# Optimization experiments

Hardware: AMD Instinct MI355X
Metric: run time of the kernel (lower is better)

Reference implementation:

```python
import jax, jax.numpy as jnp
import numpy as np

N_STEPS = 2
MAX_STEP = 1.0
EPS64 = float(np.finfo(np.float64).eps)


def _sphere_log(p, q):
    # log map on unit sphere, tangent at p pointing to q; p,q: [..., D]
    cos = jnp.clip(jnp.sum(p * q, axis=-1, keepdims=True), -1.0, 1.0)
    u = q - cos * p
    un = jnp.linalg.norm(u, axis=-1, keepdims=True)
    theta = jnp.arccos(cos)
    return theta * u / (un + 1e-12)


def _sphere_exp(p, v):
    # exp map on unit sphere; jnp.sinc(n/pi) = sin(n)/n (stable at 0)
    n = jnp.linalg.norm(v, axis=-1, keepdims=True)
    x = jnp.cos(n) * p + jnp.sinc(n / jnp.pi) * v
    return x / jnp.linalg.norm(x, axis=-1, keepdims=True)


def setup_inputs() -> dict:
    key = jax.random.key(0)
    ks = jax.random.split(key, 6)
    N, C, D, E = 50000, 16, 3, 1600000
    nodes = jax.random.normal(ks[0], (N, C, D), dtype=jnp.float32)
    nodes = nodes / jnp.linalg.norm(nodes, axis=-1, keepdims=True)  # points on S^2
    edge_w = jax.random.uniform(ks[1], (E,), dtype=jnp.float32)
    senders = jax.random.randint(ks[2], (E,), 0, N, dtype=jnp.int32)
    receivers = jax.random.randint(ks[3], (E,), 0, N, dtype=jnp.int32)
    t_sqrt = 1.0 + 0.3 * jax.random.normal(ks[4], (C,), dtype=jnp.float32)
    delta_sqrt = 1.0 + 0.3 * jax.random.normal(ks[5], (C,), dtype=jnp.float32)
    return {"nodes": nodes, "edge_w": edge_w, "t_sqrt": t_sqrt,
            "delta_sqrt": delta_sqrt, "senders": senders, "receivers": receivers}


def reference(nodes, edge_w, t_sqrt, delta_sqrt, senders, receivers):
    N = nodes.shape[0]
    t = (t_sqrt ** 2) / N_STEPS            # per-channel time, split across Euler steps
    delta = delta_sqrt ** 2                 # per-channel min step size
    deg = jax.ops.segment_sum(edge_w, senders, num_segments=N)  # [N]

    def laplace(x):
        # graph Laplacian of manifold-valued signal: weighted mean of log maps, negated
        logs = _sphere_log(x[senders], x[receivers])              # [E, C, D]
        agg = jax.ops.segment_sum(edge_w[:, None, None] * logs, senders, num_segments=N)
        return -agg / (deg[:, None, None] + 1e-12)                # [N, C, D]

    def step(x, _):
        v = laplace(x)
        nrm = jnp.sqrt(jnp.sum(v * v, axis=-1) + EPS64)           # [N, C]
        alp = jax.nn.sigmoid(nrm - delta[None, :])
        scale = jnp.where(nrm * alp <= MAX_STEP, alp, MAX_STEP / nrm)
        v = -(v * scale[..., None]) * t[None, :, None]
        return _sphere_exp(x, v), None

    x, _ = jax.lax.scan(step, nodes, None, length=N_STEPS, unroll=N_STEPS)
    return x
```

## Files before the change

kernel.cpp:

```cpp
#include <hip/hip_runtime.h>
#include <math.h>


constexpr float EPS64F = 2.2204460492503131e-16f;
constexpr float PI_F   = 3.14159265358979323846f;
constexpr int   SR_BITS = 14;
constexpr int   CH_BITS = 15;

typedef int      vi4 __attribute__((ext_vector_type(4)));
typedef float    vf4 __attribute__((ext_vector_type(4)));
typedef float    vf2 __attribute__((ext_vector_type(2)));
typedef _Float16 vh4 __attribute__((ext_vector_type(4)));


__global__ __launch_bounds__(256) void lhist_kernel(
    const int* __restrict__ snd, unsigned char* __restrict__ pos,
    unsigned char* __restrict__ partial2, int E, int NC) {
  __shared__ int h[1 << SR_BITS];
  int tid = threadIdx.x;
  int c = blockIdx.x, s = blockIdx.y;
  for (int i = tid; i < (1 << SR_BITS); i += 256) h[i] = 0;
  __syncthreads();
  int base = c << CH_BITS;
  int cnt = min(1 << CH_BITS, E - base);
  int s0 = s << SR_BITS;
  const vi4* snd4 = (const vi4*)(snd + base);
  int cnt4 = cnt >> 2;
  for (int i = tid; i < cnt4; i += 256) {
    vi4 sv = snd4[i];
    int e = base + (i << 2);
    int v;
    v = sv.x - s0; if ((unsigned)v < (1u << SR_BITS)) pos[e]     = (unsigned char)atomicAdd(&h[v], 1);
    v = sv.y - s0; if ((unsigned)v < (1u << SR_BITS)) pos[e + 1] = (unsigned char)atomicAdd(&h[v], 1);
    v = sv.z - s0; if ((unsigned)v < (1u << SR_BITS)) pos[e + 2] = (unsigned char)atomicAdd(&h[v], 1);
    v = sv.w - s0; if ((unsigned)v < (1u << SR_BITS)) pos[e + 3] = (unsigned char)atomicAdd(&h[v], 1);
  }
  if (tid == 0) {
    for (int i = cnt4 << 2; i < cnt; ++i) {
      int v = snd[base + i] - s0;
      if ((unsigned)v < (1u << SR_BITS))
        pos[base + i] = (unsigned char)atomicAdd(&h[v], 1);
    }
  }
  __syncthreads();
  unsigned char* dst = partial2 + ((size_t)(s * NC + c) << SR_BITS);
  for (int i = tid; i < (1 << SR_BITS); i += 256)
    dst[i] = (unsigned char)h[i];
}

__global__ __launch_bounds__(1024) void scan1A_kernel(
    const unsigned char* __restrict__ partial2, unsigned char* __restrict__ boffL,
    int* __restrict__ row_start, int* __restrict__ btot, int N, int NC) {
  __shared__ int wsum[16];
  int tid = threadIdx.x;
  int lane = tid & 63, wave = tid >> 6;
  int i = blockIdx.x * 1024 + tid;
  int vpad = 0;
  if (i < N) {
    int s = i >> SR_BITS, lv = i & ((1 << SR_BITS) - 1);
    int run = 0;
    for (int c = 0; c < NC; ++c) {
      int t = partial2[((size_t)(s * NC + c) << SR_BITS) + lv];
      boffL[(size_t)c * N + i] = (unsigned char)run;
      run += t;
    }
    vpad = (run + 15) & ~15;
  }
  int incl = vpad;
  #pragma unroll
  for (int off = 1; off < 64; off <<= 1) {
    int t = __shfl_up(incl, off, 64);
    if (lane >= off) incl += t;
  }
  if (lane == 63) wsum[wave] = incl;
  __syncthreads();
  if (wave == 0 && lane < 16) {
    int wincl = wsum[lane];
    #pragma unroll
    for (int off = 1; off < 16; off <<= 1) {
      int t = __shfl_up(wincl, off, 64);
      if (lane >= off) wincl += t;
    }
    wsum[lane] = wincl;
  }
  __syncthreads();
  int woff = (wave > 0) ? wsum[wave - 1] : 0;
  if (i < N) row_start[i] = woff + incl - vpad;
  if (tid == 0) btot[blockIdx.x] = wsum[15];
}

__global__ __launch_bounds__(256) void scanCD_kernel(
    int* __restrict__ row_start, const int* __restrict__ btot,
    const float* __restrict__ nodes, vh4* __restrict__ nodes_h4,
    int N, int nb) {
  __shared__ int bsh[64];
  int tid = threadIdx.x;
  if (tid < 64) {
    int v = (tid < nb) ? btot[tid] : 0;
    int incl = v;
    #pragma unroll
    for (int off = 1; off < 64; off <<= 1) {
      int t = __shfl_up(incl, off, 64);
      if (tid >= off) incl += t;
    }
    bsh[tid] = incl - v;
    if (blockIdx.x == 0 && tid == 63) row_start[N] = incl;
  }
  __syncthreads();
  int i = blockIdx.x * 256 + tid;
  if (i < N) row_start[i] = row_start[i] + bsh[i >> 10];
  int total = N * 16;
  for (int idx = blockIdx.x * 256 + tid; idx < total; idx += gridDim.x * 256) {
    const float* s = nodes + idx * 3;
    vh4 h = {(_Float16)s[0], (_Float16)s[1], (_Float16)s[2], (_Float16)0.f};
    nodes_h4[idx] = h;
  }
}

__global__ __launch_bounds__(256) void fill_kernel(
    const vi4* __restrict__ snd4, const vi4* __restrict__ rcv4,
    const vf4* __restrict__ ew4, const unsigned char* __restrict__ pos,
    const unsigned char* __restrict__ boffL, const int* __restrict__ row_start,
    int* __restrict__ pair,
    const int* __restrict__ snd, const int* __restrict__ rcv,
    const float* __restrict__ ew, int N, int E) {
  int tid = threadIdx.x;
  int E4 = E >> 2;
  #pragma unroll
  for (int gg = 0; gg < 2; ++gg) {
    int g = blockIdx.x * 512 + gg * 256 + tid;
    if (g < E4) {
      int e = g << 2;
      const unsigned char* bc = boffL + (size_t)(e >> CH_BITS) * N;
      vi4 s = __builtin_nontemporal_load(&snd4[g]);
      vi4 r = __builtin_nontemporal_load(&rcv4[g]);
      vf4 w = __builtin_nontemporal_load(&ew4[g]);
      unsigned pb = *(const unsigned*)(pos + e);
      int rs0 = row_start[s.x] + bc[s.x];
      int rs1 = row_start[s.y] + bc[s.y];
      int rs2 = row_start[s.z] + bc[s.z];
      int rs3 = row_start[s.w] + bc[s.w];
      unsigned e0 = ((unsigned)(int)fmaf(w.x, 32767.f, 0.5f) << 17) | (unsigned)r.x;
      unsigned e1 = ((unsigned)(int)fmaf(w.y, 32767.f, 0.5f) << 17) | (unsigned)r.y;
      unsigned e2 = ((unsigned)(int)fmaf(w.z, 32767.f, 0.5f) << 17) | (unsigned)r.z;
      unsigned e3 = ((unsigned)(int)fmaf(w.w, 32767.f, 0.5f) << 17) | (unsigned)r.w;
      pair[rs0 + (pb & 255u)]         = (int)e0;
      pair[rs1 + ((pb >> 8) & 255u)]  = (int)e1;
      pair[rs2 + ((pb >> 16) & 255u)] = (int)e2;
      pair[rs3 + (pb >> 24)]          = (int)e3;
    }
  }
  if (blockIdx.x == 0 && tid == 0) {
    for (int e = E4 << 2; e < E; ++e) {
      int sn = snd[e];
      pair[row_start[sn] + boffL[(size_t)(e >> CH_BITS) * N + sn] + pos[e]] =
          (int)(((unsigned)(int)fmaf(ew[e], 32767.f, 0.5f) << 17) | (unsigned)rcv[e]);
    }
  }
}


__device__ __forceinline__ void edge_accum_pk(
    vf2 p0, vf2 p1, vf2 p2, vf2 q0, vf2 q1, vf2 q2, vf2 w,
    vf2& a0, vf2& a1, vf2& a2) {
  vf2 cs = p0 * q0 + p1 * q1 + p2 * q2;
  cs = __builtin_elementwise_min(vf2{1.f, 1.f},
       __builtin_elementwise_max(vf2{-1.f, -1.f}, cs));
  vf2 u0 = q0 - cs * p0;
  vf2 u1 = q1 - cs * p1;
  vf2 u2 = q2 - cs * p2;
  vf2 un2 = __builtin_elementwise_max(u0 * u0 + u1 * u1 + u2 * u2,
                                      vf2{1e-24f, 1e-24f});
  vf2 ax = __builtin_elementwise_abs(cs);
  vf2 s = __builtin_elementwise_sqrt(vf2{1.f, 1.f} - ax);
  vf2 poly = ((ax * -0.0187293f + 0.0742610f) * ax - 0.2121144f) * ax
             + 1.5707288f;
  vf2 th = s * poly;
  vf2 theta;
  theta.x = (cs.x >= 0.0f) ? th.x : (PI_F - th.x);
  theta.y = (cs.y >= 0.0f) ? th.y : (PI_F - th.y);
  vf2 rsq;
  rsq.x = __builtin_amdgcn_rsqf(un2.x);
  rsq.y = __builtin_amdgcn_rsqf(un2.y);
  vf2 coef = w * theta * rsq;
  a0 += coef * u0;
  a1 += coef * u1;
  a2 += coef * u2;
}

__device__ __forceinline__ void node_step(
    float a0, float a1, float a2, float ws, float p0, float p1, float p2,
    float ts, float dsv, float& y0, float& y1, float& y2) {
  float invdg = __builtin_amdgcn_rcpf(ws + 1e-12f);
  float g0 = a0 * invdg, g1 = a1 * invdg, g2 = a2 * invdg;
  float nrm = sqrtf(fmaf(g0, g0, fmaf(g1, g1, g2 * g2)) + EPS64F);
  float tch = ts * ts * 0.5f;
  float dch = dsv * dsv;
  float alp = __builtin_amdgcn_rcpf(1.0f + __expf(dch - nrm));
  float scale = (nrm * alp <= 1.0f) ? alp : __builtin_amdgcn_rcpf(nrm);
  float f = scale * tch;
  float v0 = g0 * f, v1 = g1 * f, v2 = g2 * f;
  float nv = sqrtf(fmaf(v0, v0, fmaf(v1, v1, v2 * v2)));
  float cn = __cosf(nv);
  float sc = (nv > 1e-20f) ? (__sinf(nv) * __builtin_amdgcn_rcpf(nv)) : 1.0f;
  float t0 = fmaf(cn, p0, sc * v0);
  float t1 = fmaf(cn, p1, sc * v1);
  float t2 = fmaf(cn, p2, sc * v2);
  float inv = __builtin_amdgcn_rsqf(fmaf(t0, t0, fmaf(t1, t1, t2 * t2)));
  y0 = t0 * inv; y1 = t1 * inv; y2 = t2 * inv;
}

__global__ __launch_bounds__(256, 8) void flowp_kernel(
    const vh4* __restrict__ xh4, const float* __restrict__ pf,
    const int* __restrict__ row_start, const int* __restrict__ pair,
    const float* __restrict__ tsq, const float* __restrict__ dsq,
    float* __restrict__ of, vh4* __restrict__ oh4, int N) {
  int node = blockIdx.x * 4 + (threadIdx.x >> 6);
  if (node >= N) return;
  int lane = threadIdx.x & 63;
  int c = lane & 15;
  int k = lane >> 4;
  int c3 = c * 3;
  int beg = row_start[node];
  int end = row_start[node + 1];
  int ip = node * 48 + c3;
  float ps0 = pf[ip], ps1 = pf[ip + 1], ps2 = pf[ip + 2];
  vf2 p0 = {ps0, ps0}, p1 = {ps1, ps1}, p2 = {ps2, ps2};
  vf2 a0 = {0.f, 0.f}, a1 = {0.f, 0.f}, a2 = {0.f, 0.f}, wsv = {0.f, 0.f};
  int iters = (end - beg) >> 4;
  int j = beg + k;
  constexpr float WS = 1.0f / 32767.0f;
  for (int t = 0; t < iters; ++t, j += 16) {
    int e0 = __builtin_nontemporal_load(&pair[j]);
    int e1 = __builtin_nontemporal_load(&pair[j + 4]);
    int e2 = __builtin_nontemporal_load(&pair[j + 8]);
    int e3 = __builtin_nontemporal_load(&pair[j + 12]);
    float w0 = (float)((unsigned)e0 >> 17) * WS;
    float w1 = (float)((unsigned)e1 >> 17) * WS;
    float w2 = (float)((unsigned)e2 >> 17) * WS;
    float w3 = (float)((unsigned)e3 >> 17) * WS;
    vh4 qva = xh4[((e0 & 0x1FFFF) << 4) + c];
    vh4 qvb = xh4[((e1 & 0x1FFFF) << 4) + c];
    vh4 qvc = xh4[((e2 & 0x1FFFF) << 4) + c];
    vh4 qvd = xh4[((e3 & 0x1FFFF) << 4) + c];
    float qa0 = (float)qva.x, qa1 = (float)qva.y, qa2 = (float)qva.z;
    float qb0 = (float)qvb.x, qb1 = (float)qvb.y, qb2 = (float)qvb.z;
    float qc0 = (float)qvc.x, qc1 = (float)qvc.y, qc2 = (float)qvc.z;
    float qd0 = (float)qvd.x, qd1 = (float)qvd.y, qd2 = (float)qvd.z;
    vf2 wA = {w0, w1}, wB = {w2, w3};
    edge_accum_pk(p0, p1, p2, vf2{qa0, qb0}, vf2{qa1, qb1},
                  vf2{qa2, qb2}, wA, a0, a1, a2);
    edge_accum_pk(p0, p1, p2, vf2{qc0, qd0}, vf2{qc1, qd1},
                  vf2{qc2, qd2}, wB, a0, a1, a2);
    wsv += wA + wB;
  }
  float A0 = a0.x + a0.y, A1 = a1.x + a1.y, A2 = a2.x + a2.y;
  float ws = wsv.x + wsv.y;
  A0 += __shfl_xor(A0, 16); A1 += __shfl_xor(A1, 16);
  A2 += __shfl_xor(A2, 16); ws += __shfl_xor(ws, 16);
  A0 += __shfl_xor(A0, 32); A1 += __shfl_xor(A1, 32);
  A2 += __shfl_xor(A2, 32); ws += __shfl_xor(ws, 32);
  if (k == 0) {
    float y0, y1, y2;
    node_step(A0, A1, A2, ws, ps0, ps1, ps2, tsq[c], dsq[c], y0, y1, y2);
    of[ip] = y0; of[ip + 1] = y1; of[ip + 2] = y2;
    if (oh4) {
      vh4 h = {(_Float16)y0, (_Float16)y1, (_Float16)y2, (_Float16)0.f};
      oh4[node * 16 + c] = h;
    }
  }
}

static inline size_t al16(size_t x) { return (x + 15) & ~(size_t)15; }

extern "C" void kernel_launch(void* const* d_in, const int* in_sizes, int n_in,
                              void* d_out, int out_size, void* d_ws, size_t ws_size,
                              hipStream_t stream) {
  const float* nodes = (const float*)d_in[0];
  const float* ew    = (const float*)d_in[1];
  const float* tsq   = (const float*)d_in[2];
  const float* dsq   = (const float*)d_in[3];
  const int*   snd   = (const int*)d_in[4];
  const int*   rcv   = (const int*)d_in[5];
  float* out = (float*)d_out;

  int E = in_sizes[1];
  int N = in_sizes[0] / 48;

  int NS = (N + (1 << SR_BITS) - 1) >> SR_BITS;
  int NC = (E + (1 << CH_BITS) - 1) >> CH_BITS;

  size_t padN  = (size_t)E + 15 * (size_t)N + 64;
  size_t rsB   = al16((size_t)(N + 4) * 4);
  size_t auxB  = 512;
  size_t pairB = al16(padN * 4);
  size_t p2B   = al16((size_t)NS * NC << SR_BITS);
  size_t xh4B  = al16((size_t)N * 16 * 8);
  size_t boffB = al16((size_t)NC * N * 4);
  if (p2B + boffB < 2 * xh4B) boffB = 2 * xh4B - p2B;

  char* base = (char*)d_ws;
  int*           row_start = (int*)base;
  int*           btot      = (int*)(base + rsB);
  int*           pair      = (int*)(base + rsB + auxB);
  unsigned char* partial2  = (unsigned char*)(base + rsB + auxB + pairB);
  unsigned char* boffL     = partial2 + p2B;
  unsigned char* pos       = boffL + boffB;
  vh4*           xtmp_h4   = (vh4*)partial2;
  vh4*           nodes_h4  = (vh4*)(partial2 + xh4B);

  int E4  = E >> 2;
  int nb  = (N + 1023) / 1024;
  int nb2 = (N + 255) / 256;
  int fbk = (E4 + 511) / 512;
  int nfb = (N + 3) / 4;

  hipMemsetAsync(pair, 0, pairB, stream);
  lhist_kernel<<<dim3(NC, NS), 256, 0, stream>>>(snd, pos, partial2, E, NC);
  scan1A_kernel<<<nb, 1024, 0, stream>>>(partial2, boffL, row_start, btot, N, NC);
  scanCD_kernel<<<nb2, 256, 0, stream>>>(row_start, btot, nodes, nodes_h4, N, nb);
  fill_kernel<<<fbk, 256, 0, stream>>>((const vi4*)snd, (const vi4*)rcv,
                                       (const vf4*)ew, pos, boffL, row_start,
                                       pair, snd, rcv, ew, N, E);

  flowp_kernel<<<nfb, 256, 0, stream>>>(nodes_h4, nodes, row_start, pair,
                                        tsq, dsq, out, xtmp_h4, N);
  flowp_kernel<<<nfb, 256, 0, stream>>>(xtmp_h4, out, row_start, pair,
                                        tsq, dsq, out, nullptr, N);
}
```

Measured before the change: 270.9 us.

## Merge preprocessing kernels, shrink CSR padding, encode weights as fp16

Drops the separate memset and scanCD launches. Pair zeroing and the fp16 node conversion move into the histogram kernel, and the block-offset scan moves into the last block of scan1A through an atomic ticket. Consumers add bshG per 1024-node block instead of using rewritten row_start. Row padding falls from 16 to 8, and the flow kernel now processes 2 edges per iteration instead of 4. Edge weights are packed as fp16 with a 16-bit receiver index, which limits N to 65536, and unroll 2 compensates for the smaller loop body.

After: 285.2 us. 5.3% more time.

```diff
diff --git a/kernel.cpp b/kernel.cpp
--- a/kernel.cpp
+++ b/kernel.cpp
@@ -15,7 +15,10 @@
 
 __global__ __launch_bounds__(256) void lhist_kernel(
     const int* __restrict__ snd, unsigned char* __restrict__ pos,
-    unsigned char* __restrict__ partial2, int E, int NC) {
+    unsigned char* __restrict__ partial2, int E, int NC,
+    vi4* __restrict__ pairz, int pairW4,
+    const float* __restrict__ nodes, vh4* __restrict__ nodes_h4,
+    int N, int* __restrict__ ticket) {
   __shared__ int h[1 << SR_BITS];
   int tid = threadIdx.x;
   int c = blockIdx.x, s = blockIdx.y;
@@ -46,11 +49,24 @@
   unsigned char* dst = partial2 + ((size_t)(s * NC + c) << SR_BITS);
   for (int i = tid; i < (1 << SR_BITS); i += 256)
     dst[i] = (unsigned char)h[i];
+  int lb = blockIdx.y * gridDim.x + blockIdx.x;
+  int nthr = gridDim.x * gridDim.y * 256;
+  int gtid = lb * 256 + tid;
+  if (gtid == 0) *ticket = 0;
+  vi4 z = {0, 0, 0, 0};
+  for (int i = gtid; i < pairW4; i += nthr) pairz[i] = z;
+  int total = N * 16;
+  for (int idx = gtid; idx < total; idx += nthr) {
+    const float* sp = nodes + idx * 3;
+    vh4 hh = {(_Float16)sp[0], (_Float16)sp[1], (_Float16)sp[2], (_Float16)0.f};
+    nodes_h4[idx] = hh;
+  }
 }
 
 __global__ __launch_bounds__(1024) void scan1A_kernel(
     const unsigned char* __restrict__ partial2, unsigned char* __restrict__ boffL,
-    int* __restrict__ row_start, int* __restrict__ btot, int N, int NC) {
+    int* __restrict__ row_start, int* __restrict__ btot,
+    int* __restrict__ ticket, int* __restrict__ bshG, int N, int NC) {
   __shared__ int wsum[16];
   int tid = threadIdx.x;
   int lane = tid & 63, wave = tid >> 6;
@@ -64,7 +80,7 @@
       boffL[(size_t)c * N + i] = (unsigned char)run;
       run += t;
     }
-    vpad = (run + 15) & ~15;
+    vpad = (run + 7) & ~7;
   }
   int incl = vpad;
   #pragma unroll
@@ -85,35 +101,26 @@
   }
   __syncthreads();
   int woff = (wave > 0) ? wsum[wave - 1] : 0;
-  if (i < N) row_start[i] = woff + incl - vpad;
+  if (i <= N) row_start[i] = woff + incl - vpad;
   if (tid == 0) btot[blockIdx.x] = wsum[15];
-}
-
-__global__ __launch_bounds__(256) void scanCD_kernel(
-    int* __restrict__ row_start, const int* __restrict__ btot,
-    const float* __restrict__ nodes, vh4* __restrict__ nodes_h4,
-    int N, int nb) {
-  __shared__ int bsh[64];
-  int tid = threadIdx.x;
-  if (tid < 64) {
-    int v = (tid < nb) ? btot[tid] : 0;
-    int incl = v;
-    #pragma unroll
-    for (int off = 1; off < 64; off <<= 1) {
-      int t = __shfl_up(incl, off, 64);
-      if (tid >= off) incl += t;
-    }
-    bsh[tid] = incl - v;
-    if (blockIdx.x == 0 && tid == 63) row_start[N] = incl;
-  }
-  __syncthreads();
-  int i = blockIdx.x * 256 + tid;
-  if (i < N) row_start[i] = row_start[i] + bsh[i >> 10];
-  int total = N * 16;
-  for (int idx = blockIdx.x * 256 + tid; idx < total; idx += gridDim.x * 256) {
-    const float* s = nodes + idx * 3;
-    vh4 h = {(_Float16)s[0], (_Float16)s[1], (_Float16)s[2], (_Float16)0.f};
-    nodes_h4[idx] = h;
+  __threadfence();
+  __shared__ int lastFlag;
+  if (tid == 0) lastFlag = (atomicAdd(ticket, 1) == (int)gridDim.x - 1);
+  __syncthreads();
+  if (lastFlag) {
+    __threadfence();
+    if (tid < 64) {
+      int nbk = (int)gridDim.x;
+      int v = (tid < nbk) ? ((volatile int*)btot)[tid] : 0;
+      int ic = v;
+      #pragma unroll
+      for (int off = 1; off < 64; off <<= 1) {
+        int t = __shfl_up(ic, off, 64);
+        if (tid >= off) ic += t;
+      }
+      bshG[tid] = ic - v;
+    }
+    if (tid == 0 && (N & 1023) == 0) row_start[N] = 0;
   }
 }
 
@@ -121,7 +128,7 @@
     const vi4* __restrict__ snd4, const vi4* __restrict__ rcv4,
     const vf4* __restrict__ ew4, const unsigned char* __restrict__ pos,
     const unsigned char* __restrict__ boffL, const int* __restrict__ row_start,
-    int* __restrict__ pair,
+    const int* __restrict__ bshG, int* __restrict__ pair,
     const int* __restrict__ snd, const int* __restrict__ rcv,
     const float* __restrict__ ew, int N, int E) {
   int tid = threadIdx.x;
@@ -136,14 +143,14 @@
       vi4 r = __builtin_nontemporal_load(&rcv4[g]);
       vf4 w = __builtin_nontemporal_load(&ew4[g]);
       unsigned pb = *(const unsigned*)(pos + e);
-      int rs0 = row_start[s.x] + bc[s.x];
-      int rs1 = row_start[s.y] + bc[s.y];
-      int rs2 = row_start[s.z] + bc[s.z];
-      int rs3 = row_start[s.w] + bc[s.w];
-      unsigned e0 = ((unsigned)(int)fmaf(w.x, 32767.f, 0.5f) << 17) | (unsigned)r.x;
-      unsigned e1 = ((unsigned)(int)fmaf(w.y, 32767.f, 0.5f) << 17) | (unsigned)r.y;
-      unsigned e2 = ((unsigned)(int)fmaf(w.z, 32767.f, 0.5f) << 17) | (unsigned)r.z;
-      unsigned e3 = ((unsigned)(int)fmaf(w.w, 32767.f, 0.5f) << 17) | (unsigned)r.w;
+      int rs0 = row_start[s.x] + bshG[s.x >> 10] + bc[s.x];
+      int rs1 = row_start[s.y] + bshG[s.y >> 10] + bc[s.y];
+      int rs2 = row_start[s.z] + bshG[s.z >> 10] + bc[s.z];
+      int rs3 = row_start[s.w] + bshG[s.w >> 10] + bc[s.w];
+      unsigned e0 = ((unsigned)__builtin_bit_cast(unsigned short, (_Float16)w.x) << 16) | (unsigned)r.x;
+      unsigned e1 = ((unsigned)__builtin_bit_cast(unsigned short, (_Float16)w.y) << 16) | (unsigned)r.y;
+      unsigned e2 = ((unsigned)__builtin_bit_cast(unsigned short, (_Float16)w.z) << 16) | (unsigned)r.z;
+      unsigned e3 = ((unsigned)__builtin_bit_cast(unsigned short, (_Float16)w.w) << 16) | (unsigned)r.w;
       pair[rs0 + (pb & 255u)]         = (int)e0;
       pair[rs1 + ((pb >> 8) & 255u)]  = (int)e1;
       pair[rs2 + ((pb >> 16) & 255u)] = (int)e2;
@@ -153,8 +160,8 @@
   if (blockIdx.x == 0 && tid == 0) {
     for (int e = E4 << 2; e < E; ++e) {
       int sn = snd[e];
-      pair[row_start[sn] + boffL[(size_t)(e >> CH_BITS) * N + sn] + pos[e]] =
-          (int)(((unsigned)(int)fmaf(ew[e], 32767.f, 0.5f) << 17) | (unsigned)rcv[e]);
+      pair[row_start[sn] + bshG[sn >> 10] + boffL[(size_t)(e >> CH_BITS) * N + sn] + pos[e]] =
+          (int)(((unsigned)__builtin_bit_cast(unsigned short, (_Float16)ew[e]) << 16) | (unsigned)rcv[e]);
     }
   }
 }
@@ -164,14 +171,13 @@
     vf2 p0, vf2 p1, vf2 p2, vf2 q0, vf2 q1, vf2 q2, vf2 w,
     vf2& a0, vf2& a1, vf2& a2) {
   vf2 cs = p0 * q0 + p1 * q1 + p2 * q2;
-  cs = __builtin_elementwise_min(vf2{1.f, 1.f},
-       __builtin_elementwise_max(vf2{-1.f, -1.f}, cs));
+  vf2 ax = __builtin_elementwise_min(__builtin_elementwise_abs(cs),
+                                     vf2{1.f, 1.f});
   vf2 u0 = q0 - cs * p0;
   vf2 u1 = q1 - cs * p1;
   vf2 u2 = q2 - cs * p2;
   vf2 un2 = __builtin_elementwise_max(u0 * u0 + u1 * u1 + u2 * u2,
                                       vf2{1e-24f, 1e-24f});
-  vf2 ax = __builtin_elementwise_abs(cs);
   vf2 s = __builtin_elementwise_sqrt(vf2{1.f, 1.f} - ax);
   vf2 poly = ((ax * -0.0187293f + 0.0742610f) * ax - 0.2121144f) * ax
              + 1.5707288f;
@@ -212,47 +218,41 @@
 
 __global__ __launch_bounds__(256, 8) void flowp_kernel(
     const vh4* __restrict__ xh4, const float* __restrict__ pf,
-    const int* __restrict__ row_start, const int* __restrict__ pair,
-    const float* __restrict__ tsq, const float* __restrict__ dsq,
-    float* __restrict__ of, vh4* __restrict__ oh4, int N) {
+    const int* __restrict__ row_start, const int* __restrict__ bshG,
+    const int* __restrict__ pair, const float* __restrict__ tsq,
+    const float* __restrict__ dsq, float* __restrict__ of,
+    vh4* __restrict__ oh4, int N) {
   int node = blockIdx.x * 4 + (threadIdx.x >> 6);
   if (node >= N) return;
   int lane = threadIdx.x & 63;
   int c = lane & 15;
   int k = lane >> 4;
   int c3 = c * 3;
-  int beg = row_start[node];
-  int end = row_start[node + 1];
+  int beg = row_start[node] + bshG[node >> 10];
+  int end = row_start[node + 1] + bshG[(node + 1) >> 10];
   int ip = node * 48 + c3;
   float ps0 = pf[ip], ps1 = pf[ip + 1], ps2 = pf[ip + 2];
   vf2 p0 = {ps0, ps0}, p1 = {ps1, ps1}, p2 = {ps2, ps2};
   vf2 a0 = {0.f, 0.f}, a1 = {0.f, 0.f}, a2 = {0.f, 0.f}, wsv = {0.f, 0.f};
-  int iters = (end - beg) >> 4;
+  const vh4* __restrict__ xc = xh4 + c;
+  int iters = (end - beg) >> 3;
   int j = beg + k;
-  constexpr float WS = 1.0f / 32767.0f;
-  for (int t = 0; t < iters; ++t, j += 16) {
-    int e0 = __builtin_nontemporal_load(&pair[j]);
-    int e1 = __builtin_nontemporal_load(&pair[j + 4]);
-    int e2 = __builtin_nontemporal_load(&pair[j + 8]);
-    int e3 = __builtin_nontemporal_load(&pair[j + 12]);
-    float w0 = (float)((unsigned)e0 >> 17) * WS;
-    float w1 = (float)((unsigned)e1 >> 17) * WS;
-    float w2 = (float)((unsigned)e2 >> 17) * WS;
-    float w3 = (float)((unsigned)e3 >> 17) * WS;
-    vh4 qva = xh4[((e0 & 0x1FFFF) << 4) + c];
-    vh4 qvb = xh4[((e1 & 0x1FFFF) << 4) + c];
-    vh4 qvc = xh4[((e2 & 0x1FFFF) << 4) + c];
-    vh4 qvd = xh4[((e3 & 0x1FFFF) << 4) + c];
+  #pragma unroll 2
+  for (int t = 0; t < iters; ++t, j += 8) {
+    int e0 = pair[j];
+    int e1 = pair[j + 4];
+    float w0 = (float)__builtin_bit_cast(_Float16,
+                   (unsigned short)((unsigned)e0 >> 16));
+    float w1 = (float)__builtin_bit_cast(_Float16,
+                   (unsigned short)((unsigned)e1 >> 16));
+    vh4 qva = xc[(e0 & 0xFFFF) << 4];
+    vh4 qvb = xc[(e1 & 0xFFFF) << 4];
     float qa0 = (float)qva.x, qa1 = (float)qva.y, qa2 = (float)qva.z;
     float qb0 = (float)qvb.x, qb1 = (float)qvb.y, qb2 = (float)qvb.z;
-    float qc0 = (float)qvc.x, qc1 = (float)qvc.y, qc2 = (float)qvc.z;
-    float qd0 = (float)qvd.x, qd1 = (float)qvd.y, qd2 = (float)qvd.z;
-    vf2 wA = {w0, w1}, wB = {w2, w3};
+    vf2 wA = {w0, w1};
     edge_accum_pk(p0, p1, p2, vf2{qa0, qb0}, vf2{qa1, qb1},
                   vf2{qa2, qb2}, wA, a0, a1, a2);
-    edge_accum_pk(p0, p1, p2, vf2{qc0, qd0}, vf2{qc1, qd1},
-                  vf2{qc2, qd2}, wB, a0, a1, a2);
-    wsv += wA + wB;
+    wsv += wA;
   }
   float A0 = a0.x + a0.y, A1 = a1.x + a1.y, A2 = a2.x + a2.y;
   float ws = wsv.x + wsv.y;
@@ -290,9 +290,9 @@
   int NS = (N + (1 << SR_BITS) - 1) >> SR_BITS;
   int NC = (E + (1 << CH_BITS) - 1) >> CH_BITS;
 
-  size_t padN  = (size_t)E + 15 * (size_t)N + 64;
+  size_t padN  = (size_t)E + 7 * (size_t)N + 64;
   size_t rsB   = al16((size_t)(N + 4) * 4);
-  size_t auxB  = 512;
+  size_t auxB  = 768;
   size_t pairB = al16(padN * 4);
   size_t p2B   = al16((size_t)NS * NC << SR_BITS);
   size_t xh4B  = al16((size_t)N * 16 * 8);
@@ -302,6 +302,8 @@
   char* base = (char*)d_ws;
   int*           row_start = (int*)base;
   int*           btot      = (int*)(base + rsB);
+  int*           bshG      = btot + 64;
+  int*           ticket    = btot + 128;
   int*           pair      = (int*)(base + rsB + auxB);
   unsigned char* partial2  = (unsigned char*)(base + rsB + auxB + pairB);
   unsigned char* boffL     = partial2 + p2B;
@@ -311,20 +313,20 @@
 
   int E4  = E >> 2;
   int nb  = (N + 1023) / 1024;
-  int nb2 = (N + 255) / 256;
   int fbk = (E4 + 511) / 512;
   int nfb = (N + 3) / 4;
 
-  hipMemsetAsync(pair, 0, pairB, stream);
-  lhist_kernel<<<dim3(NC, NS), 256, 0, stream>>>(snd, pos, partial2, E, NC);
-  scan1A_kernel<<<nb, 1024, 0, stream>>>(partial2, boffL, row_start, btot, N, NC);
-  scanCD_kernel<<<nb2, 256, 0, stream>>>(row_start, btot, nodes, nodes_h4, N, nb);
+  lhist_kernel<<<dim3(NC, NS), 256, 0, stream>>>(
+      snd, pos, partial2, E, NC, (vi4*)pair, (int)(pairB >> 4),
+      nodes, nodes_h4, N, ticket);
+  scan1A_kernel<<<nb, 1024, 0, stream>>>(partial2, boffL, row_start, btot,
+                                         ticket, bshG, N, NC);
   fill_kernel<<<fbk, 256, 0, stream>>>((const vi4*)snd, (const vi4*)rcv,
                                        (const vf4*)ew, pos, boffL, row_start,
-                                       pair, snd, rcv, ew, N, E);
-
-  flowp_kernel<<<nfb, 256, 0, stream>>>(nodes_h4, nodes, row_start, pair,
-                                        tsq, dsq, out, xtmp_h4, N);
-  flowp_kernel<<<nfb, 256, 0, stream>>>(xtmp_h4, out, row_start, pair,
-                                        tsq, dsq, out, nullptr, N);
-}
+                                       bshG, pair, snd, rcv, ew, N, E);
+
+  flowp_kernel<<<nfb, 256, 0, stream>>>(nodes_h4, nodes, row_start, bshG,
+                                        pair, tsq, dsq, out, xtmp_h4, N);
+  flowp_kernel<<<nfb, 256, 0, stream>>>(xtmp_h4, out, row_start, bshG,
+                                        pair, tsq, dsq, out, nullptr, N);
+}
```

## Split each node across two waves and pad CSR rows to eight

Applied to the files above, without the earlier changes.

The flow kernel now gives each node two waves that take alternating 8-edge chunks and combine their partial sums through shared memory. This replaces the earlier single wave per node that handled 16 edges per step. CSR rows are padded to a multiple of 8 instead of 16, which cuts the zero-weight padding edges that still have to be gathered and computed. The packed edge word now stores a 16-bit weight and a 16-bit receiver index, so node count must stay below 65536. The split adds a block barrier and LDS traffic, lowers per-thread ILP, and drops the nontemporal hints on edge loads.

Result: slower. 284.7 us (+5.1%).

```diff
diff --git a/kernel.cpp b/kernel.cpp
--- a/kernel.cpp
+++ b/kernel.cpp
@@ -64,7 +64,7 @@
       boffL[(size_t)c * N + i] = (unsigned char)run;
       run += t;
     }
-    vpad = (run + 15) & ~15;
+    vpad = (run + 7) & ~7;
   }
   int incl = vpad;
   #pragma unroll
@@ -140,10 +140,10 @@
       int rs1 = row_start[s.y] + bc[s.y];
       int rs2 = row_start[s.z] + bc[s.z];
       int rs3 = row_start[s.w] + bc[s.w];
-      unsigned e0 = ((unsigned)(int)fmaf(w.x, 32767.f, 0.5f) << 17) | (unsigned)r.x;
-      unsigned e1 = ((unsigned)(int)fmaf(w.y, 32767.f, 0.5f) << 17) | (unsigned)r.y;
-      unsigned e2 = ((unsigned)(int)fmaf(w.z, 32767.f, 0.5f) << 17) | (unsigned)r.z;
-      unsigned e3 = ((unsigned)(int)fmaf(w.w, 32767.f, 0.5f) << 17) | (unsigned)r.w;
+      unsigned e0 = ((unsigned)(int)fmaf(w.x, 65535.f, 0.5f) << 16) | (unsigned)r.x;
+      unsigned e1 = ((unsigned)(int)fmaf(w.y, 65535.f, 0.5f) << 16) | (unsigned)r.y;
+      unsigned e2 = ((unsigned)(int)fmaf(w.z, 65535.f, 0.5f) << 16) | (unsigned)r.z;
+      unsigned e3 = ((unsigned)(int)fmaf(w.w, 65535.f, 0.5f) << 16) | (unsigned)r.w;
       pair[rs0 + (pb & 255u)]         = (int)e0;
       pair[rs1 + ((pb >> 8) & 255u)]  = (int)e1;
       pair[rs2 + ((pb >> 16) & 255u)] = (int)e2;
@@ -154,7 +154,7 @@
     for (int e = E4 << 2; e < E; ++e) {
       int sn = snd[e];
       pair[row_start[sn] + boffL[(size_t)(e >> CH_BITS) * N + sn] + pos[e]] =
-          (int)(((unsigned)(int)fmaf(ew[e], 32767.f, 0.5f) << 17) | (unsigned)rcv[e]);
+          (int)(((unsigned)(int)fmaf(ew[e], 65535.f, 0.5f) << 16) | (unsigned)rcv[e]);
     }
   }
 }
@@ -215,44 +215,44 @@
     const int* __restrict__ row_start, const int* __restrict__ pair,
     const float* __restrict__ tsq, const float* __restrict__ dsq,
     float* __restrict__ of, vh4* __restrict__ oh4, int N) {
-  int node = blockIdx.x * 4 + (threadIdx.x >> 6);
-  if (node >= N) return;
-  int lane = threadIdx.x & 63;
+  __shared__ float lred[2][16][4];
+  int tid = threadIdx.x;
+  int wave = tid >> 6;
+  int ln   = wave >> 1;
+  int sub  = wave & 1;
+  int node = blockIdx.x * 2 + ln;
+  bool active = node < N;
+  int lane = tid & 63;
   int c = lane & 15;
   int k = lane >> 4;
   int c3 = c * 3;
-  int beg = row_start[node];
-  int end = row_start[node + 1];
-  int ip = node * 48 + c3;
-  float ps0 = pf[ip], ps1 = pf[ip + 1], ps2 = pf[ip + 2];
+  int beg = 0, end = 0, ip = 0;
+  float ps0 = 0.f, ps1 = 0.f, ps2 = 0.f;
+  if (active) {
+    beg = row_start[node];
+    end = row_start[node + 1];
+    ip = node * 48 + c3;
+    ps0 = pf[ip]; ps1 = pf[ip + 1]; ps2 = pf[ip + 2];
+  }
   vf2 p0 = {ps0, ps0}, p1 = {ps1, ps1}, p2 = {ps2, ps2};
   vf2 a0 = {0.f, 0.f}, a1 = {0.f, 0.f}, a2 = {0.f, 0.f}, wsv = {0.f, 0.f};
-  int iters = (end - beg) >> 4;
-  int j = beg + k;
-  constexpr float WS = 1.0f / 32767.0f;
-  for (int t = 0; t < iters; ++t, j += 16) {
-    int e0 = __builtin_nontemporal_load(&pair[j]);
-    int e1 = __builtin_nontemporal_load(&pair[j + 4]);
-    int e2 = __builtin_nontemporal_load(&pair[j + 8]);
-    int e3 = __builtin_nontemporal_load(&pair[j + 12]);
-    float w0 = (float)((unsigned)e0 >> 17) * WS;
-    float w1 = (float)((unsigned)e1 >> 17) * WS;
-    float w2 = (float)((unsigned)e2 >> 17) * WS;
-    float w3 = (float)((unsigned)e3 >> 17) * WS;
-    vh4 qva = xh4[((e0 & 0x1FFFF) << 4) + c];
-    vh4 qvb = xh4[((e1 & 0x1FFFF) << 4) + c];
-    vh4 qvc = xh4[((e2 & 0x1FFFF) << 4) + c];
-    vh4 qvd = xh4[((e3 & 0x1FFFF) << 4) + c];
+  const vh4* __restrict__ xc = xh4 + c;
+  int T = (end - beg) >> 3;
+  int j = beg + (sub << 3) + k;
+  constexpr float WS = 1.0f / 65535.0f;
+  for (int t = sub; t < T; t += 2, j += 16) {
+    int e0 = pair[j];
+    int e1 = pair[j + 4];
+    float w0 = (float)((unsigned)e0 >> 16) * WS;
+    float w1 = (float)((unsigned)e1 >> 16) * WS;
+    vh4 qva = xc[(e0 & 0xFFFF) << 4];
+    vh4 qvb = xc[(e1 & 0xFFFF) << 4];
     float qa0 = (float)qva.x, qa1 = (float)qva.y, qa2 = (float)qva.z;
     float qb0 = (float)qvb.x, qb1 = (float)qvb.y, qb2 = (float)qvb.z;
-    float qc0 = (float)qvc.x, qc1 = (float)qvc.y, qc2 = (float)qvc.z;
-    float qd0 = (float)qvd.x, qd1 = (float)qvd.y, qd2 = (float)qvd.z;
-    vf2 wA = {w0, w1}, wB = {w2, w3};
+    vf2 wA = {w0, w1};
     edge_accum_pk(p0, p1, p2, vf2{qa0, qb0}, vf2{qa1, qb1},
                   vf2{qa2, qb2}, wA, a0, a1, a2);
-    edge_accum_pk(p0, p1, p2, vf2{qc0, qd0}, vf2{qc1, qd1},
-                  vf2{qc2, qd2}, wB, a0, a1, a2);
-    wsv += wA + wB;
+    wsv += wA;
   }
   float A0 = a0.x + a0.y, A1 = a1.x + a1.y, A2 = a2.x + a2.y;
   float ws = wsv.x + wsv.y;
@@ -260,7 +260,14 @@
   A2 += __shfl_xor(A2, 16); ws += __shfl_xor(ws, 16);
   A0 += __shfl_xor(A0, 32); A1 += __shfl_xor(A1, 32);
   A2 += __shfl_xor(A2, 32); ws += __shfl_xor(ws, 32);
-  if (k == 0) {
+  if (sub == 1 && k == 0) {
+    lred[ln][c][0] = A0; lred[ln][c][1] = A1;
+    lred[ln][c][2] = A2; lred[ln][c][3] = ws;
+  }
+  __syncthreads();
+  if (active && sub == 0 && k == 0) {
+    A0 += lred[ln][c][0]; A1 += lred[ln][c][1];
+    A2 += lred[ln][c][2]; ws += lred[ln][c][3];
     float y0, y1, y2;
     node_step(A0, A1, A2, ws, ps0, ps1, ps2, tsq[c], dsq[c], y0, y1, y2);
     of[ip] = y0; of[ip + 1] = y1; of[ip + 2] = y2;
@@ -290,7 +297,7 @@
   int NS = (N + (1 << SR_BITS) - 1) >> SR_BITS;
   int NC = (E + (1 << CH_BITS) - 1) >> CH_BITS;
 
-  size_t padN  = (size_t)E + 15 * (size_t)N + 64;
+  size_t padN  = (size_t)E + 7 * (size_t)N + 64;
   size_t rsB   = al16((size_t)(N + 4) * 4);
   size_t auxB  = 512;
   size_t pairB = al16(padN * 4);
@@ -313,7 +320,7 @@
   int nb  = (N + 1023) / 1024;
   int nb2 = (N + 255) / 256;
   int fbk = (E4 + 511) / 512;
-  int nfb = (N + 3) / 4;
+  int nfb = (N + 1) / 2;
 
   hipMemsetAsync(pair, 0, pairB, stream);
   lhist_kernel<<<dim3(NC, NS), 256, 0, stream>>>(snd, pos, partial2, E, NC);
```

## Replace chunked histogram CSR build with atomic degree count and cursor fill

Applied to the files above, without the earlier changes.

Replaces the chunk-local shared-memory histogram, per-chunk offset scan, and deterministic placement with a global atomic degree count, an exclusive scan, and an atomic-cursor scatter fill. The padding per row drops from 16 to 8 and the flow kernel processes two edges per lane per iteration with unroll 2 instead of four. The packed edge word now uses a 16-bit receiver index and a 16-bit weight. This removes the large byte arrays and one kernel pass but relies on global atomics with random contention. Edge order within a row becomes nondeterministic, and 16-bit receiver indices only cover N up to 65536.

After: 376.0 us. +38.8%, slower.

```diff
diff --git a/kernel.cpp b/kernel.cpp
--- a/kernel.cpp
+++ b/kernel.cpp
@@ -4,8 +4,6 @@
 
 constexpr float EPS64F = 2.2204460492503131e-16f;
 constexpr float PI_F   = 3.14159265358979323846f;
-constexpr int   SR_BITS = 14;
-constexpr int   CH_BITS = 15;
 
 typedef int      vi4 __attribute__((ext_vector_type(4)));
 typedef float    vf4 __attribute__((ext_vector_type(4)));
@@ -13,59 +11,30 @@
 typedef _Float16 vh4 __attribute__((ext_vector_type(4)));
 
 
-__global__ __launch_bounds__(256) void lhist_kernel(
-    const int* __restrict__ snd, unsigned char* __restrict__ pos,
-    unsigned char* __restrict__ partial2, int E, int NC) {
-  __shared__ int h[1 << SR_BITS];
-  int tid = threadIdx.x;
-  int c = blockIdx.x, s = blockIdx.y;
-  for (int i = tid; i < (1 << SR_BITS); i += 256) h[i] = 0;
-  __syncthreads();
-  int base = c << CH_BITS;
-  int cnt = min(1 << CH_BITS, E - base);
-  int s0 = s << SR_BITS;
-  const vi4* snd4 = (const vi4*)(snd + base);
-  int cnt4 = cnt >> 2;
-  for (int i = tid; i < cnt4; i += 256) {
-    vi4 sv = snd4[i];
-    int e = base + (i << 2);
-    int v;
-    v = sv.x - s0; if ((unsigned)v < (1u << SR_BITS)) pos[e]     = (unsigned char)atomicAdd(&h[v], 1);
-    v = sv.y - s0; if ((unsigned)v < (1u << SR_BITS)) pos[e + 1] = (unsigned char)atomicAdd(&h[v], 1);
-    v = sv.z - s0; if ((unsigned)v < (1u << SR_BITS)) pos[e + 2] = (unsigned char)atomicAdd(&h[v], 1);
-    v = sv.w - s0; if ((unsigned)v < (1u << SR_BITS)) pos[e + 3] = (unsigned char)atomicAdd(&h[v], 1);
-  }
-  if (tid == 0) {
-    for (int i = cnt4 << 2; i < cnt; ++i) {
-      int v = snd[base + i] - s0;
-      if ((unsigned)v < (1u << SR_BITS))
-        pos[base + i] = (unsigned char)atomicAdd(&h[v], 1);
-    }
-  }
-  __syncthreads();
-  unsigned char* dst = partial2 + ((size_t)(s * NC + c) << SR_BITS);
-  for (int i = tid; i < (1 << SR_BITS); i += 256)
-    dst[i] = (unsigned char)h[i];
-}
-
-__global__ __launch_bounds__(1024) void scan1A_kernel(
-    const unsigned char* __restrict__ partial2, unsigned char* __restrict__ boffL,
-    int* __restrict__ row_start, int* __restrict__ btot, int N, int NC) {
+__global__ __launch_bounds__(256) void degree_kernel(
+    const vi4* __restrict__ snd4, int* __restrict__ deg,
+    const int* __restrict__ snd, int E) {
+  int E4 = E >> 2;
+  for (int g = blockIdx.x * 256 + threadIdx.x; g < E4; g += gridDim.x * 256) {
+    vi4 s = __builtin_nontemporal_load(&snd4[g]);
+    atomicAdd(&deg[s.x], 1);
+    atomicAdd(&deg[s.y], 1);
+    atomicAdd(&deg[s.z], 1);
+    atomicAdd(&deg[s.w], 1);
+  }
+  if (blockIdx.x == 0 && threadIdx.x == 0) {
+    for (int e = E4 << 2; e < E; ++e) atomicAdd(&deg[snd[e]], 1);
+  }
+}
+
+__global__ __launch_bounds__(1024) void scanP_kernel(
+    const int* __restrict__ deg, int* __restrict__ row_start,
+    int* __restrict__ btot, int N) {
   __shared__ int wsum[16];
   int tid = threadIdx.x;
   int lane = tid & 63, wave = tid >> 6;
   int i = blockIdx.x * 1024 + tid;
-  int vpad = 0;
-  if (i < N) {
-    int s = i >> SR_BITS, lv = i & ((1 << SR_BITS) - 1);
-    int run = 0;
-    for (int c = 0; c < NC; ++c) {
-      int t = partial2[((size_t)(s * NC + c) << SR_BITS) + lv];
-      boffL[(size_t)c * N + i] = (unsigned char)run;
-      run += t;
-    }
-    vpad = (run + 15) & ~15;
-  }
+  int vpad = (i < N) ? ((deg[i] + 7) & ~7) : 0;
   int incl = vpad;
   #pragma unroll
   for (int off = 1; off < 64; off <<= 1) {
@@ -89,10 +58,10 @@
   if (tid == 0) btot[blockIdx.x] = wsum[15];
 }
 
-__global__ __launch_bounds__(256) void scanCD_kernel(
-    int* __restrict__ row_start, const int* __restrict__ btot,
-    const float* __restrict__ nodes, vh4* __restrict__ nodes_h4,
-    int N, int nb) {
+__global__ __launch_bounds__(256) void scanF_kernel(
+    int* __restrict__ row_start, int* __restrict__ cursor,
+    const int* __restrict__ btot, const float* __restrict__ nodes,
+    vh4* __restrict__ nodes_h4, int N, int nb) {
   __shared__ int bsh[64];
   int tid = threadIdx.x;
   if (tid < 64) {
@@ -108,7 +77,11 @@
   }
   __syncthreads();
   int i = blockIdx.x * 256 + tid;
-  if (i < N) row_start[i] = row_start[i] + bsh[i >> 10];
+  if (i < N) {
+    int rs = row_start[i] + bsh[i >> 10];
+    row_start[i] = rs;
+    cursor[i] = rs;
+  }
   int total = N * 16;
   for (int idx = blockIdx.x * 256 + tid; idx < total; idx += gridDim.x * 256) {
     const float* s = nodes + idx * 3;
@@ -117,44 +90,29 @@
   }
 }
 
-__global__ __launch_bounds__(256) void fill_kernel(
+__global__ __launch_bounds__(256) void fillA_kernel(
     const vi4* __restrict__ snd4, const vi4* __restrict__ rcv4,
-    const vf4* __restrict__ ew4, const unsigned char* __restrict__ pos,
-    const unsigned char* __restrict__ boffL, const int* __restrict__ row_start,
-    int* __restrict__ pair,
-    const int* __restrict__ snd, const int* __restrict__ rcv,
-    const float* __restrict__ ew, int N, int E) {
-  int tid = threadIdx.x;
+    const vf4* __restrict__ ew4, int* __restrict__ cursor,
+    int* __restrict__ pair, const int* __restrict__ snd,
+    const int* __restrict__ rcv, const float* __restrict__ ew, int E) {
   int E4 = E >> 2;
-  #pragma unroll
-  for (int gg = 0; gg < 2; ++gg) {
-    int g = blockIdx.x * 512 + gg * 256 + tid;
-    if (g < E4) {
-      int e = g << 2;
-      const unsigned char* bc = boffL + (size_t)(e >> CH_BITS) * N;
-      vi4 s = __builtin_nontemporal_load(&snd4[g]);
-      vi4 r = __builtin_nontemporal_load(&rcv4[g]);
-      vf4 w = __builtin_nontemporal_load(&ew4[g]);
-      unsigned pb = *(const unsigned*)(pos + e);
-      int rs0 = row_start[s.x] + bc[s.x];
-      int rs1 = row_start[s.y] + bc[s.y];
-      int rs2 = row_start[s.z] + bc[s.z];
-      int rs3 = row_start[s.w] + bc[s.w];
-      unsigned e0 = ((unsigned)(int)fmaf(w.x, 32767.f, 0.5f) << 17) | (unsigned)r.x;
-      unsigned e1 = ((unsigned)(int)fmaf(w.y, 32767.f, 0.5f) << 17) | (unsigned)r.y;
-      unsigned e2 = ((unsigned)(int)fmaf(w.z, 32767.f, 0.5f) << 17) | (unsigned)r.z;
-      unsigned e3 = ((unsigned)(int)fmaf(w.w, 32767.f, 0.5f) << 17) | (unsigned)r.w;
-      pair[rs0 + (pb & 255u)]         = (int)e0;
-      pair[rs1 + ((pb >> 8) & 255u)]  = (int)e1;
-      pair[rs2 + ((pb >> 16) & 255u)] = (int)e2;
-      pair[rs3 + (pb >> 24)]          = (int)e3;
-    }
-  }
-  if (blockIdx.x == 0 && tid == 0) {
+  for (int g = blockIdx.x * 256 + threadIdx.x; g < E4; g += gridDim.x * 256) {
+    vi4 s = __builtin_nontemporal_load(&snd4[g]);
+    vi4 r = __builtin_nontemporal_load(&rcv4[g]);
+    vf4 w = __builtin_nontemporal_load(&ew4[g]);
+    int p0 = atomicAdd(&cursor[s.x], 1);
+    int p1 = atomicAdd(&cursor[s.y], 1);
+    int p2 = atomicAdd(&cursor[s.z], 1);
+    int p3 = atomicAdd(&cursor[s.w], 1);
+    pair[p0] = (int)(((unsigned)(int)fmaf(w.x, 65535.f, 0.5f) << 16) | (unsigned)r.x);
+    pair[p1] = (int)(((unsigned)(int)fmaf(w.y, 65535.f, 0.5f) << 16) | (unsigned)r.y);
+    pair[p2] = (int)(((unsigned)(int)fmaf(w.z, 65535.f, 0.5f) << 16) | (unsigned)r.z);
+    pair[p3] = (int)(((unsigned)(int)fmaf(w.w, 65535.f, 0.5f) << 16) | (unsigned)r.w);
+  }
+  if (blockIdx.x == 0 && threadIdx.x == 0) {
     for (int e = E4 << 2; e < E; ++e) {
-      int sn = snd[e];
-      pair[row_start[sn] + boffL[(size_t)(e >> CH_BITS) * N + sn] + pos[e]] =
-          (int)(((unsigned)(int)fmaf(ew[e], 32767.f, 0.5f) << 17) | (unsigned)rcv[e]);
+      int p = atomicAdd(&cursor[snd[e]], 1);
+      pair[p] = (int)(((unsigned)(int)fmaf(ew[e], 65535.f, 0.5f) << 16) | (unsigned)rcv[e]);
     }
   }
 }
@@ -227,32 +185,24 @@
   float ps0 = pf[ip], ps1 = pf[ip + 1], ps2 = pf[ip + 2];
   vf2 p0 = {ps0, ps0}, p1 = {ps1, ps1}, p2 = {ps2, ps2};
   vf2 a0 = {0.f, 0.f}, a1 = {0.f, 0.f}, a2 = {0.f, 0.f}, wsv = {0.f, 0.f};
-  int iters = (end - beg) >> 4;
+  const vh4* __restrict__ xc = xh4 + c;
+  int iters = (end - beg) >> 3;
   int j = beg + k;
-  constexpr float WS = 1.0f / 32767.0f;
-  for (int t = 0; t < iters; ++t, j += 16) {
-    int e0 = __builtin_nontemporal_load(&pair[j]);
-    int e1 = __builtin_nontemporal_load(&pair[j + 4]);
-    int e2 = __builtin_nontemporal_load(&pair[j + 8]);
-    int e3 = __builtin_nontemporal_load(&pair[j + 12]);
-    float w0 = (float)((unsigned)e0 >> 17) * WS;
-    float w1 = (float)((unsigned)e1 >> 17) * WS;
-    float w2 = (float)((unsigned)e2 >> 17) * WS;
-    float w3 = (float)((unsigned)e3 >> 17) * WS;
-    vh4 qva = xh4[((e0 & 0x1FFFF) << 4) + c];
-    vh4 qvb = xh4[((e1 & 0x1FFFF) << 4) + c];
-    vh4 qvc = xh4[((e2 & 0x1FFFF) << 4) + c];
-    vh4 qvd = xh4[((e3 & 0x1FFFF) << 4) + c];
+  constexpr float WS = 1.0f / 65535.0f;
+  #pragma unroll 2
+  for (int t = 0; t < iters; ++t, j += 8) {
+    int e0 = pair[j];
+    int e1 = pair[j + 4];
+    float w0 = (float)((unsigned)e0 >> 16) * WS;
+    float w1 = (float)((unsigned)e1 >> 16) * WS;
+    vh4 qva = xc[(e0 & 0xFFFF) << 4];
+    vh4 qvb = xc[(e1 & 0xFFFF) << 4];
     float qa0 = (float)qva.x, qa1 = (float)qva.y, qa2 = (float)qva.z;
     float qb0 = (float)qvb.x, qb1 = (float)qvb.y, qb2 = (float)qvb.z;
-    float qc0 = (float)qvc.x, qc1 = (float)qvc.y, qc2 = (float)qvc.z;
-    float qd0 = (float)qvd.x, qd1 = (float)qvd.y, qd2 = (float)qvd.z;
-    vf2 wA = {w0, w1}, wB = {w2, w3};
+    vf2 wA = {w0, w1};
     edge_accum_pk(p0, p1, p2, vf2{qa0, qb0}, vf2{qa1, qb1},
                   vf2{qa2, qb2}, wA, a0, a1, a2);
-    edge_accum_pk(p0, p1, p2, vf2{qc0, qd0}, vf2{qc1, qd1},
-                  vf2{qc2, qd2}, wB, a0, a1, a2);
-    wsv += wA + wB;
+    wsv += wA;
   }
   float A0 = a0.x + a0.y, A1 = a1.x + a1.y, A2 = a2.x + a2.y;
   float ws = wsv.x + wsv.y;
@@ -287,41 +237,36 @@
   int E = in_sizes[1];
   int N = in_sizes[0] / 48;
 
-  int NS = (N + (1 << SR_BITS) - 1) >> SR_BITS;
-  int NC = (E + (1 << CH_BITS) - 1) >> CH_BITS;
-
-  size_t padN  = (size_t)E + 15 * (size_t)N + 64;
-  size_t rsB   = al16((size_t)(N + 4) * 4);
-  size_t auxB  = 512;
+  size_t padN  = (size_t)E + 7 * (size_t)N + 64;
+  size_t rsB   = al16((size_t)(N + 8) * 4);
+  size_t curB  = al16((size_t)N * 4);
   size_t pairB = al16(padN * 4);
-  size_t p2B   = al16((size_t)NS * NC << SR_BITS);
+  size_t degB  = al16((size_t)N * 4 + 256);
   size_t xh4B  = al16((size_t)N * 16 * 8);
-  size_t boffB = al16((size_t)NC * N * 4);
-  if (p2B + boffB < 2 * xh4B) boffB = 2 * xh4B - p2B;
 
   char* base = (char*)d_ws;
-  int*           row_start = (int*)base;
-  int*           btot      = (int*)(base + rsB);
-  int*           pair      = (int*)(base + rsB + auxB);
-  unsigned char* partial2  = (unsigned char*)(base + rsB + auxB + pairB);
-  unsigned char* boffL     = partial2 + p2B;
-  unsigned char* pos       = boffL + boffB;
-  vh4*           xtmp_h4   = (vh4*)partial2;
-  vh4*           nodes_h4  = (vh4*)(partial2 + xh4B);
+  int* row_start = (int*)base;
+  int* cursor    = (int*)(base + rsB);
+  int* pair      = (int*)(base + rsB + curB);
+  int* deg       = (int*)(base + rsB + curB + pairB);
+  int* btot      = deg + N;
+  vh4* nodes_h4  = (vh4*)(base + rsB + curB + pairB + degB);
+  vh4* xtmp_h4   = (vh4*)(base + rsB + curB + pairB + degB + xh4B);
 
   int E4  = E >> 2;
   int nb  = (N + 1023) / 1024;
   int nb2 = (N + 255) / 256;
-  int fbk = (E4 + 511) / 512;
+  int egb = (E4 + 255) / 256;
   int nfb = (N + 3) / 4;
 
-  hipMemsetAsync(pair, 0, pairB, stream);
-  lhist_kernel<<<dim3(NC, NS), 256, 0, stream>>>(snd, pos, partial2, E, NC);
-  scan1A_kernel<<<nb, 1024, 0, stream>>>(partial2, boffL, row_start, btot, N, NC);
-  scanCD_kernel<<<nb2, 256, 0, stream>>>(row_start, btot, nodes, nodes_h4, N, nb);
-  fill_kernel<<<fbk, 256, 0, stream>>>((const vi4*)snd, (const vi4*)rcv,
-                                       (const vf4*)ew, pos, boffL, row_start,
-                                       pair, snd, rcv, ew, N, E);
+  hipMemsetAsync(pair, 0, pairB + degB, stream);
+  degree_kernel<<<egb, 256, 0, stream>>>((const vi4*)snd, deg, snd, E);
+  scanP_kernel<<<nb, 1024, 0, stream>>>(deg, row_start, btot, N);
+  scanF_kernel<<<nb2, 256, 0, stream>>>(row_start, cursor, btot,
+                                        nodes, nodes_h4, N, nb);
+  fillA_kernel<<<egb, 256, 0, stream>>>((const vi4*)snd, (const vi4*)rcv,
+                                        (const vf4*)ew, cursor, pair,
+                                        snd, rcv, ew, E);
 
   flowp_kernel<<<nfb, 256, 0, stream>>>(nodes_h4, nodes, row_start, pair,
                                         tsq, dsq, out, xtmp_h4, N);
```
